# Performance work log

Measured on AMD Instinct MI355X. Metric: run time of the kernel, lower is better.

The kernel has to match this reference:

```python
import jax, jax.numpy as jnp
import numpy as np

N_NODES = 50000
N_EDGES = 800000
IN_DIM = 128
HEADS1, D1 = 4, 16   # hidden_dim // 4 = 16, concat -> 64
HID = HEADS1 * D1    # 64
OUT_DIM = 40
NEG_SLOPE = 0.2      # PyG GATConv default


def setup_inputs() -> dict:
    key = jax.random.key(0)
    ks = jax.random.split(key, 11)
    x = jax.random.normal(ks[0], (N_NODES, IN_DIM), dtype=jnp.float32)
    edge_index = jax.random.randint(ks[1], (2, N_EDGES), 0, N_NODES)
    s1 = 1.0 / np.sqrt(IN_DIM)
    s2 = 1.0 / np.sqrt(HID)
    return {
        "x": x,
        "edge_index": edge_index,
        "W1": jax.random.normal(ks[2], (IN_DIM, HEADS1 * D1), dtype=jnp.float32) * s1,
        "a_src1": jax.random.normal(ks[3], (HEADS1, D1), dtype=jnp.float32) * s2,
        "a_dst1": jax.random.normal(ks[4], (HEADS1, D1), dtype=jnp.float32) * s2,
        "b1": jnp.zeros((HID,), dtype=jnp.float32),
        "W2": jax.random.normal(ks[5], (HID, OUT_DIM), dtype=jnp.float32) * s2,
        "a_src2": jax.random.normal(ks[6], (1, OUT_DIM), dtype=jnp.float32) * s2,
        "a_dst2": jax.random.normal(ks[7], (1, OUT_DIM), dtype=jnp.float32) * s2,
        "b2": jnp.zeros((OUT_DIM,), dtype=jnp.float32),
    }


def gat_conv(x, src, dst, W, a_src, a_dst, b, heads, d, n_nodes):
    # linear projection, split into heads: [N, H, d]
    h = (x @ W).reshape(n_nodes, heads, d)
    # per-node attention logits: [N, H]
    alpha_src = jnp.einsum("nhd,hd->nh", h, a_src)
    alpha_dst = jnp.einsum("nhd,hd->nh", h, a_dst)
    # edge attention coefficients
    e = jax.nn.leaky_relu(alpha_src[src] + alpha_dst[dst], NEG_SLOPE)  # [E, H]
    # segment softmax over incoming edges of each destination node
    e_max = jax.ops.segment_max(e, dst, num_segments=n_nodes)
    e_max = jnp.where(jnp.isfinite(e_max), e_max, 0.0)
    e_exp = jnp.exp(e - e_max[dst])
    denom = jax.ops.segment_sum(e_exp, dst, num_segments=n_nodes)
    alpha = e_exp / (denom[dst] + 1e-16)  # [E, H]
    # weighted scatter-aggregate of source messages
    out = jax.ops.segment_sum(h[src] * alpha[..., None], dst, num_segments=n_nodes)
    return out.reshape(n_nodes, heads * d) + b


def reference(x, edge_index, W1, a_src1, a_dst1, b1, W2, a_src2, a_dst2, b2):
    n = x.shape[0]
    # PyG GATConv add_self_loops=True
    loop = jnp.arange(n, dtype=edge_index.dtype)
    src = jnp.concatenate([edge_index[0], loop])
    dst = jnp.concatenate([edge_index[1], loop])
    h = jax.nn.relu(gat_conv(x, src, dst, W1, a_src1, a_dst1, b1, HEADS1, D1, n))
    # dropout is identity in eval mode
    h = gat_conv(h, src, dst, W2, a_src2, a_dst2, b2, 1, OUT_DIM, n)
    return jax.nn.log_softmax(h, axis=1)
```

## Files before the change

kernel.cpp:

```cpp
#include <hip/hip_runtime.h>
#include <hip/hip_fp16.h>
#include <math.h>

#define NN    50000
#define NE0   800000
#define NE    850000
#define INDIM 128
#define HID   64
#define OUTD  40

#define NB    391
#define BSH   7
#define BCAP  3072

typedef unsigned short u16;
typedef unsigned char  u8;

__device__ inline u16 f2bf(float f) {
    unsigned u = __float_as_uint(f);
    return (u16)((u + 0x8000u) >> 16);
}
__device__ inline float bf2f(u16 h) {
    return __uint_as_float((unsigned)h << 16);
}

__global__ __launch_bounds__(512) void k_binit(int* __restrict__ bcur) {
    int i = threadIdx.x;
    if (i < NB) bcur[i] = i * BCAP;
}

__global__ __launch_bounds__(256) void k_bin(const int* __restrict__ ei,
                                             int* __restrict__ bcur,
                                             unsigned int* __restrict__ epack) {
    __shared__ int lh[NB];
    __shared__ int lbase[NB];
    const int tid = threadIdx.x;
    const int CH = (NE + 255) / 256;
    const int e_begin = blockIdx.x * CH;
    const int e_end = (e_begin + CH < NE) ? e_begin + CH : NE;

    for (int i = tid; i < NB; i += 256) lh[i] = 0;
    __syncthreads();
    for (int e = e_begin + tid; e < e_end; e += 256) {
        int dst = (e < NE0) ? ei[NE0 + e] : (e - NE0);
        atomicAdd(&lh[dst >> BSH], 1);
    }
    __syncthreads();
    for (int i = tid; i < NB; i += 256) {
        int c = lh[i];
        lbase[i] = c ? atomicAdd(&bcur[i], c) : 0;
        lh[i] = 0;
    }
    __syncthreads();
    for (int e = e_begin + tid; e < e_end; e += 256) {
        int src, dst;
        if (e < NE0) { src = ei[e]; dst = ei[NE0 + e]; }
        else         { src = e - NE0; dst = src; }
        int bkt = dst >> BSH;
        int lpos = atomicAdd(&lh[bkt], 1);
        epack[lbase[bkt] + lpos] = (unsigned int)src | ((unsigned int)(dst & 127) << 16);
    }
}

__global__ __launch_bounds__(256) void k_bucket_csr(
    const int* __restrict__ bcur, const unsigned int* __restrict__ epack,
    const float* __restrict__ asrc1, const float* __restrict__ adst1,
    int* __restrict__ off_s, int* __restrict__ off_e, int* __restrict__ esrc,
    u8* __restrict__ edst8, u16* __restrict__ w1u) {
    __shared__ int lh[128];
    __shared__ int lcur[128];
    __shared__ int sblk;
    __shared__ float sadst[512];
    const int tid = threadIdx.x, lane = tid & 63;
    const int b = blockIdx.x;
    const int e0 = b * BCAP;
    const int cnt = bcur[b] - e0;

    for (int i = tid; i < 512; i += 256) {
        int gi = b * 512 + i;
        sadst[i] = (gi < NN * 4) ? adst1[gi] : 0.f;
    }
    if (tid < 128) lh[tid] = 0;
    __syncthreads();
    for (int i = tid; i < cnt; i += 256)
        atomicAdd(&lh[epack[e0 + i] >> 16], 1);
    __syncthreads();

    int v = 0, incl = 0;
    if (tid < 128) {
        v = lh[tid];
        incl = v;
#pragma unroll
        for (int s = 1; s < 64; s <<= 1) {
            int t = __shfl_up(incl, s);
            if (lane >= s) incl += t;
        }
    }
    if (tid == 63) sblk = incl;
    __syncthreads();
    if (tid >= 64 && tid < 128) incl += sblk;
    if (tid < 128) {
        int ex = e0 + incl - v;
        lcur[tid] = ex;
        int gd = b * 128 + tid;
        if (gd < NN) { off_s[gd] = ex; off_e[gd] = ex + v; }
    }
    __syncthreads();

    for (int i = tid; i < cnt; i += 256) {
        unsigned int p = epack[e0 + i];
        int s  = (int)(p & 0xFFFFu);
        int dl = (int)(p >> 16);
        int pos = atomicAdd(&lcur[dl], 1);
        esrc[pos]  = s;
        edst8[pos] = (u8)dl;
        float4 av = *(const float4*)&asrc1[(size_t)s * 4];
        const float* ad = &sadst[dl * 4];
        float e0f = av.x + ad[0], e1f = av.y + ad[1];
        float e2f = av.z + ad[2], e3f = av.w + ad[3];
        e0f = (e0f > 0.f) ? e0f : 0.2f * e0f;
        e1f = (e1f > 0.f) ? e1f : 0.2f * e1f;
        e2f = (e2f > 0.f) ? e2f : 0.2f * e2f;
        e3f = (e3f > 0.f) ? e3f : 0.2f * e3f;
        unsigned lo = (unsigned)f2bf(__expf(e0f)) | ((unsigned)f2bf(__expf(e1f)) << 16);
        unsigned hi = (unsigned)f2bf(__expf(e2f)) | ((unsigned)f2bf(__expf(e3f)) << 16);
        *(uint2*)&w1u[(size_t)pos * 4] = make_uint2(lo, hi);
    }
}

__global__ __launch_bounds__(256) void k_w2(
    const int* __restrict__ bcur, const int* __restrict__ esrc,
    const u8* __restrict__ edst8, const float* __restrict__ asrc2,
    const float* __restrict__ adst2, u16* __restrict__ w2u) {
    __shared__ float sadst[128];
    const int tid = threadIdx.x;
    const int b = blockIdx.x;
    const int e0 = b * BCAP, e1 = bcur[b];
    if (tid < 128) {
        int gd = b * 128 + tid;
        sadst[tid] = (gd < NN) ? adst2[gd] : 0.f;
    }
    __syncthreads();
    for (int i = e0 + tid; i < e1; i += 256) {
        int s = esrc[i];
        float e = asrc2[s] + sadst[edst8[i]];
        e = (e > 0.f) ? e : 0.2f * e;
        w2u[i] = f2bf(__expf(e));
    }
}

__global__ __launch_bounds__(256, 2) void k_gemm1(
    const float* __restrict__ x, const float* __restrict__ W1,
    const float* __restrict__ a_s, const float* __restrict__ a_d,
    __half* __restrict__ h1h, float* __restrict__ asrc1, float* __restrict__ adst1)
{
    __shared__ float Wl[INDIM * HID];
    __shared__ float xs[64 * 132];
    const int tid = threadIdx.x;
    const int r0 = blockIdx.x * 64;

    const float4* W4 = (const float4*)W1;
    float4* Wl4 = (float4*)Wl;
#pragma unroll
    for (int i = 0; i < 8; ++i) Wl4[tid + i * 256] = W4[tid + i * 256];

    const float4* x4 = (const float4*)x;
#pragma unroll
    for (int i = 0; i < 8; ++i) {
        int idx = tid + i * 256;
        int row = idx >> 5;
        int k4  = idx & 31;
        int nr = r0 + row;
        float4 v = make_float4(0.f, 0.f, 0.f, 0.f);
        if (nr < NN) v = x4[(size_t)nr * 32 + k4];
        *(float4*)&xs[row * 132 + k4 * 4] = v;
    }
    __syncthreads();

    const int rg = tid >> 4;
    const int cg = tid & 15;
    const int c4 = cg * 4;
    const float as0 = a_s[c4], as1v = a_s[c4+1], as2v = a_s[c4+2], as3v = a_s[c4+3];
    const float ad0 = a_d[c4], ad1v = a_d[c4+1], ad2v = a_d[c4+2], ad3v = a_d[c4+3];

    float acc[4][4];
#pragma unroll
    for (int i = 0; i < 4; ++i)
#pragma unroll
        for (int j = 0; j < 4; ++j) acc[i][j] = 0.f;

#pragma unroll 4
    for (int k4 = 0; k4 < 32; ++k4) {
        float4 xv[4];
#pragma unroll
        for (int i = 0; i < 4; ++i)
            xv[i] = *(const float4*)&xs[(rg * 4 + i) * 132 + k4 * 4];
        const float* wp = &Wl[(k4 * 4) * HID + c4];
        float4 w0 = *(const float4*)(wp);
        float4 w1 = *(const float4*)(wp + HID);
        float4 w2 = *(const float4*)(wp + 2 * HID);
        float4 w3 = *(const float4*)(wp + 3 * HID);
#pragma unroll
        for (int i = 0; i < 4; ++i) {
            acc[i][0] += xv[i].x * w0.x + xv[i].y * w1.x + xv[i].z * w2.x + xv[i].w * w3.x;
            acc[i][1] += xv[i].x * w0.y + xv[i].y * w1.y + xv[i].z * w2.y + xv[i].w * w3.y;
            acc[i][2] += xv[i].x * w0.z + xv[i].y * w1.z + xv[i].z * w2.z + xv[i].w * w3.z;
            acc[i][3] += xv[i].x * w0.w + xv[i].y * w1.w + xv[i].z * w2.w + xv[i].w * w3.w;
        }
    }

#pragma unroll
    for (int i = 0; i < 4; ++i) {
        const int n = r0 + rg * 4 + i;
        if (n < NN) {
            __half2 ha = __floats2half2_rn(acc[i][0], acc[i][1]);
            __half2 hb = __floats2half2_rn(acc[i][2], acc[i][3]);
            *(__half2*)&h1h[(size_t)n * HID + c4]     = ha;
            *(__half2*)&h1h[(size_t)n * HID + c4 + 2] = hb;
        }
        float ps = acc[i][0] * as0 + acc[i][1] * as1v + acc[i][2] * as2v + acc[i][3] * as3v;
        float pd = acc[i][0] * ad0 + acc[i][1] * ad1v + acc[i][2] * ad2v + acc[i][3] * ad3v;
        ps += __shfl_xor(ps, 1); ps += __shfl_xor(ps, 2);
        pd += __shfl_xor(pd, 1); pd += __shfl_xor(pd, 2);
        if ((cg & 3) == 0 && n < NN) {
            int head = cg >> 2;
            asrc1[n * 4 + head] = ps;
            adst1[n * 4 + head] = pd;
        }
    }
}

__global__ __launch_bounds__(256) void k_fagg1(
    const int* __restrict__ off_s, const int* __restrict__ off_e,
    const int* __restrict__ esrc, const u16* __restrict__ w1u,
    const __half* __restrict__ h1h, const float* __restrict__ b1,
    float* __restrict__ hmid)
{
    const int wv = threadIdx.x >> 6, lane = threadIdx.x & 63;
    const int g = lane >> 5, li = lane & 31;
    const int n = blockIdx.x * 8 + wv * 2 + g;
    const int s0 = off_s[n], s1 = off_e[n];
    const int hp = li >> 3;
    const int last = s1 - 1;

    int maxc = s1 - s0;
    maxc = max(maxc, __shfl_xor(maxc, 32));

    float l = 0.f, a0 = 0.f, a1 = 0.f;
    const char* h1b = (const char*)h1h;
    for (int t = 0; t < maxc; t += 8) {
        int   sx[8];
        float wx[8];
#pragma unroll
        for (int j = 0; j < 8; ++j) {
            int ix  = s0 + t + j;
            int ixc = (ix < s1) ? ix : last;
            sx[j] = esrc[ixc];
            float w = bf2f(w1u[(size_t)ixc * 4 + hp]);
            wx[j] = (ix < s1) ? w : 0.f;
        }
        float2 hx[8];
#pragma unroll
        for (int j = 0; j < 8; ++j) {
            __half2 hv = *(const __half2*)(h1b + ((size_t)sx[j] * 128 + li * 4));
            hx[j] = __half22float2(hv);
        }
#pragma unroll
        for (int j = 0; j < 8; ++j) {
            l  += wx[j];
            a0 += wx[j] * hx[j].x;
            a1 += wx[j] * hx[j].y;
        }
    }
    float2 bv = *(const float2*)&b1[li * 2];
    float rcp = 1.f / l;
    float2 o;
    o.x = fmaxf(a0 * rcp + bv.x, 0.f);
    o.y = fmaxf(a1 * rcp + bv.y, 0.f);
    *(float2*)&hmid[(size_t)n * HID + li * 2] = o;
}

__global__ __launch_bounds__(320) void k_gemm2(
    const float* __restrict__ hin, const float* __restrict__ W2,
    const float* __restrict__ a_s, const float* __restrict__ a_d,
    __half* __restrict__ h2h, float* __restrict__ asrc2, float* __restrict__ adst2)
{
    __shared__ float Wl[HID * OUTD];
    __shared__ float xs[32 * 68];
    __shared__ float s_as[32], s_ad[32];
    const int tid = threadIdx.x;
    const int r0 = blockIdx.x * 32;

    const float4* W4 = (const float4*)W2;
    float4* Wl4 = (float4*)Wl;
    for (int i = tid; i < 640; i += 320) Wl4[i] = W4[i];
    const float4* x4 = (const float4*)hin;
    for (int i = tid; i < 512; i += 320) {
        int row = i >> 4;
        int k4  = i & 15;
        int nr = r0 + row;
        float4 v = make_float4(0.f, 0.f, 0.f, 0.f);
        if (nr < NN) v = x4[(size_t)nr * 16 + k4];
        *(float4*)&xs[row * 68 + k4 * 4] = v;
    }
    if (tid < 32) { s_as[tid] = 0.f; s_ad[tid] = 0.f; }
    __syncthreads();

    const int r  = tid / 10;
    const int cg = tid % 10;
    const int c4 = cg * 4;
    float a0 = 0.f, a1 = 0.f, a2 = 0.f, a3 = 0.f;
#pragma unroll 4
    for (int k4 = 0; k4 < 16; ++k4) {
        float4 xv = *(const float4*)&xs[r * 68 + k4 * 4];
        const float* wp = &Wl[(k4 * 4) * OUTD + c4];
        float4 w0 = *(const float4*)(wp);
        float4 w1 = *(const float4*)(wp + OUTD);
        float4 w2 = *(const float4*)(wp + 2 * OUTD);
        float4 w3 = *(const float4*)(wp + 3 * OUTD);
        a0 += xv.x * w0.x + xv.y * w1.x + xv.z * w2.x + xv.w * w3.x;
        a1 += xv.x * w0.y + xv.y * w1.y + xv.z * w2.y + xv.w * w3.y;
        a2 += xv.x * w0.z + xv.y * w1.z + xv.z * w2.z + xv.w * w3.z;
        a3 += xv.x * w0.w + xv.y * w1.w + xv.z * w2.w + xv.w * w3.w;
    }
    const int n = r0 + r;
    float ps = a0 * a_s[c4] + a1 * a_s[c4 + 1] + a2 * a_s[c4 + 2] + a3 * a_s[c4 + 3];
    float pd = a0 * a_d[c4] + a1 * a_d[c4 + 1] + a2 * a_d[c4 + 2] + a3 * a_d[c4 + 3];
    atomicAdd(&s_as[r], ps);
    atomicAdd(&s_ad[r], pd);
    if (n < NN) {
        __half2 ha = __floats2half2_rn(a0, a1);
        __half2 hb = __floats2half2_rn(a2, a3);
        *(__half2*)&h2h[(size_t)n * OUTD + c4]     = ha;
        *(__half2*)&h2h[(size_t)n * OUTD + c4 + 2] = hb;
    }
    __syncthreads();
    if (tid < 32) {
        int n2 = r0 + tid;
        if (n2 < NN) { asrc2[n2] = s_as[tid]; adst2[n2] = s_ad[tid]; }
    }
}

__global__ __launch_bounds__(256) void k_fagg2(
    const int* __restrict__ off_s, const int* __restrict__ off_e,
    const int* __restrict__ esrc, const u16* __restrict__ w2u,
    const __half* __restrict__ h2h, const float* __restrict__ b2,
    float* __restrict__ out)
{
    __shared__ float svals[12][OUTD];
    const int wv = threadIdx.x >> 6, lane = threadIdx.x & 63;
    const int g = lane / 20;
    const int li = lane - g * 20;
    const bool ga = (g < 3);
    const int n = blockIdx.x * 12 + wv * 3 + (ga ? g : 0);
    const bool valid = ga && (n < NN);
    const int nc = valid ? n : 0;
    const int s0 = off_s[nc], s1 = off_e[nc];
    const int last = s1 - 1;

    int maxc = valid ? (s1 - s0) : 0;
#pragma unroll
    for (int o = 1; o < 64; o <<= 1) maxc = max(maxc, __shfl_xor(maxc, o));

    float l = 0.f, a0 = 0.f, a1 = 0.f;
    const char* h2b = (const char*)h2h;
    for (int t = 0; t < maxc; t += 8) {
        int   sx[8];
        float wx[8];
#pragma unroll
        for (int j = 0; j < 8; ++j) {
            int ix  = s0 + t + j;
            int ixc = (ix < s1) ? ix : last;
            sx[j] = esrc[ixc];
            float w = bf2f(w2u[ixc]);
            wx[j] = (ix < s1) ? w : 0.f;
        }
        float2 hx[8];
#pragma unroll
        for (int j = 0; j < 8; ++j) {
            __half2 hv = *(const __half2*)(h2b + ((size_t)sx[j] * 80 + li * 4));
            hx[j] = __half22float2(hv);
        }
#pragma unroll
        for (int j = 0; j < 8; ++j) {
            l  += wx[j];
            a0 += wx[j] * hx[j].x;
            a1 += wx[j] * hx[j].y;
        }
    }
    if (valid) {
        float rcp = 1.f / l;
        float2 bv = *(const float2*)&b2[li * 2];
        svals[wv * 3 + g][li * 2]     = a0 * rcp + bv.x;
        svals[wv * 3 + g][li * 2 + 1] = a1 * rcp + bv.y;
    }
    __syncthreads();

    for (int r = wv; r < 12; r += 4) {
        int n2 = blockIdx.x * 12 + r;
        if (n2 >= NN) continue;
        float v = (lane < OUTD) ? svals[r][lane] : -1e30f;
        float mx = v;
#pragma unroll
        for (int o = 32; o; o >>= 1) mx = fmaxf(mx, __shfl_xor(mx, o));
        float ex = (lane < OUTD) ? __expf(v - mx) : 0.f;
        float sm = ex;
#pragma unroll
        for (int o = 32; o; o >>= 1) sm += __shfl_xor(sm, o);
        if (lane < OUTD) out[(size_t)n2 * OUTD + lane] = v - mx - __logf(sm);
    }
}

extern "C" void kernel_launch(void* const* d_in, const int* in_sizes, int n_in,
                              void* d_out, int out_size, void* d_ws, size_t ws_size,
                              hipStream_t stream)
{
    const float* x   = (const float*)d_in[0];
    const int*   ei  = (const int*)  d_in[1];
    const float* W1  = (const float*)d_in[2];
    const float* as1 = (const float*)d_in[3];
    const float* ad1 = (const float*)d_in[4];
    const float* b1  = (const float*)d_in[5];
    const float* W2  = (const float*)d_in[6];
    const float* as2 = (const float*)d_in[7];
    const float* ad2 = (const float*)d_in[8];
    const float* b2  = (const float*)d_in[9];
    float* out = (float*)d_out;

    char* ws = (char*)d_ws;
    __half* h1h   = (__half*)(ws);
    float*  hmid  = (float*) (ws + 6400000);
    unsigned int* epack = (unsigned int*)(ws + 6400000);
    u16*    w1u   = (u16*)   (ws + 19200000);
    __half* h2h   = (__half*)(ws + 19200000);
    float*  asrc2 = (float*) (ws + 23200000);
    float*  adst2 = (float*) (ws + 23400000);
    u16*    w2u   = (u16*)   (ws + 23600000);
    float*  asrc1 = (float*) (ws + 28809216);
    float*  adst1 = (float*) (ws + 29609216);
    int*    off_s = (int*)   (ws + 30409216);
    int*    off_e = (int*)   (ws + 30609216);
    int*    esrc  = (int*)   (ws + 30809216);
    u8*     edst8 = (u8*)    (ws + 35613824);
    int*    bcur  = (int*)   (ws + 36814976);

    hipLaunchKernelGGL(k_binit,      dim3(1),    dim3(512), 0, stream, bcur);
    hipLaunchKernelGGL(k_bin,        dim3(256),  dim3(256), 0, stream, ei, bcur, epack);
    hipLaunchKernelGGL(k_gemm1,      dim3(782),  dim3(256), 0, stream, x, W1, as1, ad1, h1h, asrc1, adst1);
    hipLaunchKernelGGL(k_bucket_csr, dim3(NB),   dim3(256), 0, stream, bcur, epack, asrc1, adst1, off_s, off_e, esrc, edst8, w1u);
    hipLaunchKernelGGL(k_fagg1,      dim3(6250), dim3(256), 0, stream, off_s, off_e, esrc, w1u, h1h, b1, hmid);
    hipLaunchKernelGGL(k_gemm2,      dim3(1563), dim3(320), 0, stream, hmid, W2, as2, ad2, h2h, asrc2, adst2);
    hipLaunchKernelGGL(k_w2,         dim3(NB),   dim3(256), 0, stream, bcur, esrc, edst8, asrc2, adst2, w2u);
    hipLaunchKernelGGL(k_fagg2,      dim3(4167), dim3(256), 0, stream, off_s, off_e, esrc, w2u, h2h, b2, out);
}
```

Baseline: 208.4 us.

## Fuse layer-2 edge weights into aggregation and pack edge records

Removes the separate k_w2 kernel: layer-2 attention weights are now computed on the fly inside k_fagg2 from asrc2/adst2, which adds a gather per edge but drops one kernel launch and a pass over the edges. Layer-1 edge data (src plus four bf16 weights) is packed into one 16-byte record, so k_fagg1 issues a single vector load per edge instead of two loads. The record is padded with an unused dst field, which raises the bytes read per edge. k_bin also uses half as many blocks, each handling a larger chunk.

Measured after the change: 212.6 us. 1.02x slower.

```diff
diff --git a/kernel.cpp b/kernel.cpp
--- a/kernel.cpp
+++ b/kernel.cpp
@@ -35,7 +35,7 @@
     __shared__ int lh[NB];
     __shared__ int lbase[NB];
     const int tid = threadIdx.x;
-    const int CH = (NE + 255) / 256;
+    const int CH = (NE + 127) / 128;
     const int e_begin = blockIdx.x * CH;
     const int e_end = (e_begin + CH < NE) ? e_begin + CH : NE;
 
@@ -65,8 +65,8 @@
 __global__ __launch_bounds__(256) void k_bucket_csr(
     const int* __restrict__ bcur, const unsigned int* __restrict__ epack,
     const float* __restrict__ asrc1, const float* __restrict__ adst1,
-    int* __restrict__ off_s, int* __restrict__ off_e, int* __restrict__ esrc,
-    u8* __restrict__ edst8, u16* __restrict__ w1u) {
+    int* __restrict__ off_s, int* __restrict__ off_e,
+    uint4* __restrict__ erec, int* __restrict__ esrc) {
     __shared__ int lh[128];
     __shared__ int lcur[128];
     __shared__ int sblk;
@@ -112,8 +112,6 @@
         int s  = (int)(p & 0xFFFFu);
         int dl = (int)(p >> 16);
         int pos = atomicAdd(&lcur[dl], 1);
-        esrc[pos]  = s;
-        edst8[pos] = (u8)dl;
         float4 av = *(const float4*)&asrc1[(size_t)s * 4];
         const float* ad = &sadst[dl * 4];
         float e0f = av.x + ad[0], e1f = av.y + ad[1];
@@ -124,28 +122,8 @@
         e3f = (e3f > 0.f) ? e3f : 0.2f * e3f;
         unsigned lo = (unsigned)f2bf(__expf(e0f)) | ((unsigned)f2bf(__expf(e1f)) << 16);
         unsigned hi = (unsigned)f2bf(__expf(e2f)) | ((unsigned)f2bf(__expf(e3f)) << 16);
-        *(uint2*)&w1u[(size_t)pos * 4] = make_uint2(lo, hi);
-    }
-}
-
-__global__ __launch_bounds__(256) void k_w2(
-    const int* __restrict__ bcur, const int* __restrict__ esrc,
-    const u8* __restrict__ edst8, const float* __restrict__ asrc2,
-    const float* __restrict__ adst2, u16* __restrict__ w2u) {
-    __shared__ float sadst[128];
-    const int tid = threadIdx.x;
-    const int b = blockIdx.x;
-    const int e0 = b * BCAP, e1 = bcur[b];
-    if (tid < 128) {
-        int gd = b * 128 + tid;
-        sadst[tid] = (gd < NN) ? adst2[gd] : 0.f;
-    }
-    __syncthreads();
-    for (int i = e0 + tid; i < e1; i += 256) {
-        int s = esrc[i];
-        float e = asrc2[s] + sadst[edst8[i]];
-        e = (e > 0.f) ? e : 0.2f * e;
-        w2u[i] = f2bf(__expf(e));
+        erec[pos] = make_uint4((unsigned)s, lo, hi, (unsigned)dl);
+        esrc[pos] = s;
     }
 }
 
@@ -232,7 +210,7 @@
 
 __global__ __launch_bounds__(256) void k_fagg1(
     const int* __restrict__ off_s, const int* __restrict__ off_e,
-    const int* __restrict__ esrc, const u16* __restrict__ w1u,
+    const uint4* __restrict__ erec,
     const __half* __restrict__ h1h, const float* __restrict__ b1,
     float* __restrict__ hmid)
 {
@@ -249,20 +227,22 @@
     float l = 0.f, a0 = 0.f, a1 = 0.f;
     const char* h1b = (const char*)h1h;
     for (int t = 0; t < maxc; t += 8) {
-        int   sx[8];
+        uint4 er[8];
         float wx[8];
 #pragma unroll
         for (int j = 0; j < 8; ++j) {
             int ix  = s0 + t + j;
             int ixc = (ix < s1) ? ix : last;
-            sx[j] = esrc[ixc];
-            float w = bf2f(w1u[(size_t)ixc * 4 + hp]);
+            er[j] = erec[ixc];
+            unsigned pair = (hp & 2) ? er[j].z : er[j].y;
+            unsigned wb = (hp & 1) ? (pair >> 16) : (pair & 0xFFFFu);
+            float w = bf2f((u16)wb);
             wx[j] = (ix < s1) ? w : 0.f;
         }
         float2 hx[8];
 #pragma unroll
         for (int j = 0; j < 8; ++j) {
-            __half2 hv = *(const __half2*)(h1b + ((size_t)sx[j] * 128 + li * 4));
+            __half2 hv = *(const __half2*)(h1b + ((size_t)er[j].x * 128 + li * 4));
             hx[j] = __half22float2(hv);
         }
 #pragma unroll
@@ -343,7 +323,8 @@
 
 __global__ __launch_bounds__(256) void k_fagg2(
     const int* __restrict__ off_s, const int* __restrict__ off_e,
-    const int* __restrict__ esrc, const u16* __restrict__ w2u,
+    const int* __restrict__ esrc, const float* __restrict__ asrc2,
+    const float* __restrict__ adst2,
     const __half* __restrict__ h2h, const float* __restrict__ b2,
     float* __restrict__ out)
 {
@@ -357,6 +338,7 @@
     const int nc = valid ? n : 0;
     const int s0 = off_s[nc], s1 = off_e[nc];
     const int last = s1 - 1;
+    const float adst = adst2[nc];
 
     int maxc = valid ? (s1 - s0) : 0;
 #pragma unroll
@@ -365,16 +347,18 @@
     float l = 0.f, a0 = 0.f, a1 = 0.f;
     const char* h2b = (const char*)h2h;
     for (int t = 0; t < maxc; t += 8) {
-        int   sx[8];
-        float wx[8];
+        int sx[8];
+        int ok[8];
 #pragma unroll
         for (int j = 0; j < 8; ++j) {
             int ix  = s0 + t + j;
-            int ixc = (ix < s1) ? ix : last;
+            ok[j] = (ix < s1);
+            int ixc = ok[j] ? ix : last;
             sx[j] = esrc[ixc];
-            float w = bf2f(w2u[ixc]);
-            wx[j] = (ix < s1) ? w : 0.f;
-        }
+        }
+        float ax[8];
+#pragma unroll
+        for (int j = 0; j < 8; ++j) ax[j] = asrc2[sx[j]];
         float2 hx[8];
 #pragma unroll
         for (int j = 0; j < 8; ++j) {
@@ -383,9 +367,13 @@
         }
 #pragma unroll
         for (int j = 0; j < 8; ++j) {
-            l  += wx[j];
-            a0 += wx[j] * hx[j].x;
-            a1 += wx[j] * hx[j].y;
+            float e = ax[j] + adst;
+            e = (e > 0.f) ? e : 0.2f * e;
+            float w = __expf(e);
+            w = ok[j] ? w : 0.f;
+            l  += w;
+            a0 += w * hx[j].x;
+            a1 += w * hx[j].y;
         }
     }
     if (valid) {
@@ -429,27 +417,24 @@
 
     char* ws = (char*)d_ws;
     __half* h1h   = (__half*)(ws);
-    float*  hmid  = (float*) (ws + 6400000);
-    unsigned int* epack = (unsigned int*)(ws + 6400000);
-    u16*    w1u   = (u16*)   (ws + 19200000);
+    float*  hmid  = (float*) (ws +  6400000);
     __half* h2h   = (__half*)(ws + 19200000);
-    float*  asrc2 = (float*) (ws + 23200000);
-    float*  adst2 = (float*) (ws + 23400000);
-    u16*    w2u   = (u16*)   (ws + 23600000);
-    float*  asrc1 = (float*) (ws + 28809216);
-    float*  adst1 = (float*) (ws + 29609216);
-    int*    off_s = (int*)   (ws + 30409216);
-    int*    off_e = (int*)   (ws + 30609216);
-    int*    esrc  = (int*)   (ws + 30809216);
-    u8*     edst8 = (u8*)    (ws + 35613824);
-    int*    bcur  = (int*)   (ws + 36814976);
+    float*  asrc1 = (float*) (ws + 23200000);
+    float*  adst1 = (float*) (ws + 24000000);
+    float*  asrc2 = (float*) (ws + 24800000);
+    float*  adst2 = (float*) (ws + 25000000);
+    int*    off_s = (int*)   (ws + 25200000);
+    int*    off_e = (int*)   (ws + 25400000);
+    unsigned int* epack = (unsigned int*)(ws + 25600000);
+    uint4*  erec  = (uint4*) (ws + 30404608);
+    int*    esrc  = (int*)   (ws + 49623040);
+    int*    bcur  = (int*)   (ws + 54427648);
 
     hipLaunchKernelGGL(k_binit,      dim3(1),    dim3(512), 0, stream, bcur);
-    hipLaunchKernelGGL(k_bin,        dim3(256),  dim3(256), 0, stream, ei, bcur, epack);
+    hipLaunchKernelGGL(k_bin,        dim3(128),  dim3(256), 0, stream, ei, bcur, epack);
     hipLaunchKernelGGL(k_gemm1,      dim3(782),  dim3(256), 0, stream, x, W1, as1, ad1, h1h, asrc1, adst1);
-    hipLaunchKernelGGL(k_bucket_csr, dim3(NB),   dim3(256), 0, stream, bcur, epack, asrc1, adst1, off_s, off_e, esrc, edst8, w1u);
-    hipLaunchKernelGGL(k_fagg1,      dim3(6250), dim3(256), 0, stream, off_s, off_e, esrc, w1u, h1h, b1, hmid);
+    hipLaunchKernelGGL(k_bucket_csr, dim3(NB),   dim3(256), 0, stream, bcur, epack, asrc1, adst1, off_s, off_e, erec, esrc);
+    hipLaunchKernelGGL(k_fagg1,      dim3(6250), dim3(256), 0, stream, off_s, off_e, erec, h1h, b1, hmid);
     hipLaunchKernelGGL(k_gemm2,      dim3(1563), dim3(320), 0, stream, hmid, W2, as2, ad2, h2h, asrc2, adst2);
-    hipLaunchKernelGGL(k_w2,         dim3(NB),   dim3(256), 0, stream, bcur, esrc, edst8, asrc2, adst2, w2u);
-    hipLaunchKernelGGL(k_fagg2,      dim3(4167), dim3(256), 0, stream, off_s, off_e, esrc, w2u, h2h, b2, out);
-}
+    hipLaunchKernelGGL(k_fagg2,      dim3(4167), dim3(256), 0, stream, off_s, off_e, esrc, asrc2, adst2, h2h, b2, out);
+}
```

## Cache edges in LDS during binning, widen aggregation lanes, store hidden in fp16

Applied to the files above, without the earlier changes.

The binning kernel now keeps each block's edge records in shared memory during the histogram pass, so edge_index is read from global memory once instead of twice. Both aggregation kernels move from 2 to 4 features per lane, so each node uses half as many lanes and each block covers twice as many nodes. The per-wavefront max-degree loop bound becomes a per-group loop bound. The intermediate hidden layer is stored as fp16 instead of fp32, halving that write and the read in the second GEMM, and the workspace is re-laid out to match. The cost is more lane divergence within a wavefront on the variable-length edge loops, fewer lanes per gather, and some rounding from the fp16 hidden layer.

Measured after the change: 208.0 us. Within noise of the previous version (-0.2%).

```diff
diff --git a/kernel.cpp b/kernel.cpp
--- a/kernel.cpp
+++ b/kernel.cpp
@@ -34,16 +34,23 @@
                                              unsigned int* __restrict__ epack) {
     __shared__ int lh[NB];
     __shared__ int lbase[NB];
+    __shared__ unsigned ebuf[3328];
     const int tid = threadIdx.x;
     const int CH = (NE + 255) / 256;
-    const int e_begin = blockIdx.x * CH;
-    const int e_end = (e_begin + CH < NE) ? e_begin + CH : NE;
+    const int e0 = blockIdx.x * CH;
+    const int e1 = (e0 + CH < NE) ? e0 + CH : NE;
+    const int cnt = e1 - e0;
 
     for (int i = tid; i < NB; i += 256) lh[i] = 0;
     __syncthreads();
-    for (int e = e_begin + tid; e < e_end; e += 256) {
-        int dst = (e < NE0) ? ei[NE0 + e] : (e - NE0);
-        atomicAdd(&lh[dst >> BSH], 1);
+    for (int i = tid; i < cnt; i += 256) {
+        int e = e0 + i;
+        int src, dst;
+        if (e < NE0) { src = ei[e]; dst = ei[NE0 + e]; }
+        else         { src = e - NE0; dst = src; }
+        int bkt = dst >> BSH;
+        ebuf[i] = (unsigned)src | ((unsigned)(dst & 127) << 16) | ((unsigned)bkt << 23);
+        atomicAdd(&lh[bkt], 1);
     }
     __syncthreads();
     for (int i = tid; i < NB; i += 256) {
@@ -52,13 +59,11 @@
         lh[i] = 0;
     }
     __syncthreads();
-    for (int e = e_begin + tid; e < e_end; e += 256) {
-        int src, dst;
-        if (e < NE0) { src = ei[e]; dst = ei[NE0 + e]; }
-        else         { src = e - NE0; dst = src; }
-        int bkt = dst >> BSH;
+    for (int i = tid; i < cnt; i += 256) {
+        unsigned rec = ebuf[i];
+        int bkt = rec >> 23;
         int lpos = atomicAdd(&lh[bkt], 1);
-        epack[lbase[bkt] + lpos] = (unsigned int)src | ((unsigned int)(dst & 127) << 16);
+        epack[lbase[bkt] + lpos] = rec & 0x7FFFFFu;
     }
 }
 
@@ -234,54 +239,60 @@
     const int* __restrict__ off_s, const int* __restrict__ off_e,
     const int* __restrict__ esrc, const u16* __restrict__ w1u,
     const __half* __restrict__ h1h, const float* __restrict__ b1,
-    float* __restrict__ hmid)
+    __half* __restrict__ hmid)
 {
     const int wv = threadIdx.x >> 6, lane = threadIdx.x & 63;
-    const int g = lane >> 5, li = lane & 31;
-    const int n = blockIdx.x * 8 + wv * 2 + g;
+    const int g = lane >> 4, li = lane & 15;
+    const int n = blockIdx.x * 16 + wv * 4 + g;
     const int s0 = off_s[n], s1 = off_e[n];
-    const int hp = li >> 3;
+    const int hp = li >> 2;
     const int last = s1 - 1;
 
-    int maxc = s1 - s0;
-    maxc = max(maxc, __shfl_xor(maxc, 32));
-
-    float l = 0.f, a0 = 0.f, a1 = 0.f;
-    const char* h1b = (const char*)h1h;
-    for (int t = 0; t < maxc; t += 8) {
+    float l = 0.f, a0 = 0.f, a1 = 0.f, a2 = 0.f, a3 = 0.f;
+    const char* hb = (const char*)h1h;
+    for (int t = s0; t < s1; t += 8) {
         int   sx[8];
         float wx[8];
 #pragma unroll
         for (int j = 0; j < 8; ++j) {
-            int ix  = s0 + t + j;
+            int ix  = t + j;
             int ixc = (ix < s1) ? ix : last;
             sx[j] = esrc[ixc];
             float w = bf2f(w1u[(size_t)ixc * 4 + hp]);
             wx[j] = (ix < s1) ? w : 0.f;
         }
-        float2 hx[8];
-#pragma unroll
-        for (int j = 0; j < 8; ++j) {
-            __half2 hv = *(const __half2*)(h1b + ((size_t)sx[j] * 128 + li * 4));
-            hx[j] = __half22float2(hv);
+        float2 f0[8], f1[8];
+#pragma unroll
+        for (int j = 0; j < 8; ++j) {
+            uint2 raw = *(const uint2*)(hb + ((size_t)sx[j] * 128 + li * 8));
+            f0[j] = __half22float2(*(__half2*)&raw.x);
+            f1[j] = __half22float2(*(__half2*)&raw.y);
         }
 #pragma unroll
         for (int j = 0; j < 8; ++j) {
             l  += wx[j];
-            a0 += wx[j] * hx[j].x;
-            a1 += wx[j] * hx[j].y;
-        }
-    }
-    float2 bv = *(const float2*)&b1[li * 2];
+            a0 += wx[j] * f0[j].x;
+            a1 += wx[j] * f0[j].y;
+            a2 += wx[j] * f1[j].x;
+            a3 += wx[j] * f1[j].y;
+        }
+    }
     float rcp = 1.f / l;
-    float2 o;
-    o.x = fmaxf(a0 * rcp + bv.x, 0.f);
-    o.y = fmaxf(a1 * rcp + bv.y, 0.f);
-    *(float2*)&hmid[(size_t)n * HID + li * 2] = o;
+    float4 bv = *(const float4*)&b1[li * 4];
+    float o0 = fmaxf(a0 * rcp + bv.x, 0.f);
+    float o1 = fmaxf(a1 * rcp + bv.y, 0.f);
+    float o2 = fmaxf(a2 * rcp + bv.z, 0.f);
+    float o3 = fmaxf(a3 * rcp + bv.w, 0.f);
+    __half2 ha = __floats2half2_rn(o0, o1);
+    __half2 hc = __floats2half2_rn(o2, o3);
+    uint2 st;
+    st.x = *(unsigned*)&ha;
+    st.y = *(unsigned*)&hc;
+    *(uint2*)((char*)hmid + ((size_t)n * 128 + li * 8)) = st;
 }
 
 __global__ __launch_bounds__(320) void k_gemm2(
-    const float* __restrict__ hin, const float* __restrict__ W2,
+    const __half* __restrict__ hin, const float* __restrict__ W2,
     const float* __restrict__ a_s, const float* __restrict__ a_d,
     __half* __restrict__ h2h, float* __restrict__ asrc2, float* __restrict__ adst2)
 {
@@ -294,14 +305,19 @@
     const float4* W4 = (const float4*)W2;
     float4* Wl4 = (float4*)Wl;
     for (int i = tid; i < 640; i += 320) Wl4[i] = W4[i];
-    const float4* x4 = (const float4*)hin;
+    const uint2* x4 = (const uint2*)hin;
     for (int i = tid; i < 512; i += 320) {
         int row = i >> 4;
-        int k4  = i & 15;
+        int c   = i & 15;
         int nr = r0 + row;
         float4 v = make_float4(0.f, 0.f, 0.f, 0.f);
-        if (nr < NN) v = x4[(size_t)nr * 16 + k4];
-        *(float4*)&xs[row * 68 + k4 * 4] = v;
+        if (nr < NN) {
+            uint2 raw = x4[(size_t)nr * 16 + c];
+            float2 p0 = __half22float2(*(__half2*)&raw.x);
+            float2 p1 = __half22float2(*(__half2*)&raw.y);
+            v = make_float4(p0.x, p0.y, p1.x, p1.y);
+        }
+        *(float4*)&xs[row * 68 + c * 4] = v;
     }
     if (tid < 32) { s_as[tid] = 0.f; s_ad[tid] = 0.f; }
     __syncthreads();
@@ -347,57 +363,59 @@
     const __half* __restrict__ h2h, const float* __restrict__ b2,
     float* __restrict__ out)
 {
-    __shared__ float svals[12][OUTD];
+    __shared__ float svals[24][OUTD];
     const int wv = threadIdx.x >> 6, lane = threadIdx.x & 63;
-    const int g = lane / 20;
-    const int li = lane - g * 20;
-    const bool ga = (g < 3);
-    const int n = blockIdx.x * 12 + wv * 3 + (ga ? g : 0);
+    const int g = lane / 10;
+    const int li = lane - g * 10;
+    const bool ga = (g < 6);
+    const int n = blockIdx.x * 24 + wv * 6 + (ga ? g : 0);
     const bool valid = ga && (n < NN);
-    const int nc = valid ? n : 0;
-    const int s0 = off_s[nc], s1 = off_e[nc];
+    const int s0 = valid ? off_s[n] : 0;
+    const int s1 = valid ? off_e[n] : 0;
     const int last = s1 - 1;
 
-    int maxc = valid ? (s1 - s0) : 0;
-#pragma unroll
-    for (int o = 1; o < 64; o <<= 1) maxc = max(maxc, __shfl_xor(maxc, o));
-
-    float l = 0.f, a0 = 0.f, a1 = 0.f;
-    const char* h2b = (const char*)h2h;
-    for (int t = 0; t < maxc; t += 8) {
+    float l = 0.f, a0 = 0.f, a1 = 0.f, a2 = 0.f, a3 = 0.f;
+    const char* hb = (const char*)h2h;
+    for (int t = s0; t < s1; t += 8) {
         int   sx[8];
         float wx[8];
 #pragma unroll
         for (int j = 0; j < 8; ++j) {
-            int ix  = s0 + t + j;
+            int ix  = t + j;
             int ixc = (ix < s1) ? ix : last;
             sx[j] = esrc[ixc];
             float w = bf2f(w2u[ixc]);
             wx[j] = (ix < s1) ? w : 0.f;
         }
-        float2 hx[8];
-#pragma unroll
-        for (int j = 0; j < 8; ++j) {
-            __half2 hv = *(const __half2*)(h2b + ((size_t)sx[j] * 80 + li * 4));
-            hx[j] = __half22float2(hv);
+        float2 f0[8], f1[8];
+#pragma unroll
+        for (int j = 0; j < 8; ++j) {
+            uint2 raw = *(const uint2*)(hb + ((size_t)sx[j] * 80 + li * 8));
+            f0[j] = __half22float2(*(__half2*)&raw.x);
+            f1[j] = __half22float2(*(__half2*)&raw.y);
         }
 #pragma unroll
         for (int j = 0; j < 8; ++j) {
             l  += wx[j];
-            a0 += wx[j] * hx[j].x;
-            a1 += wx[j] * hx[j].y;
+            a0 += wx[j] * f0[j].x;
+            a1 += wx[j] * f0[j].y;
+            a2 += wx[j] * f1[j].x;
+            a3 += wx[j] * f1[j].y;
         }
     }
     if (valid) {
         float rcp = 1.f / l;
-        float2 bv = *(const float2*)&b2[li * 2];
-        svals[wv * 3 + g][li * 2]     = a0 * rcp + bv.x;
-        svals[wv * 3 + g][li * 2 + 1] = a1 * rcp + bv.y;
-    }
-    __syncthreads();
-
-    for (int r = wv; r < 12; r += 4) {
-        int n2 = blockIdx.x * 12 + r;
+        float4 bv = *(const float4*)&b2[li * 4];
+        int r = wv * 6 + g;
+        svals[r][li * 4]     = a0 * rcp + bv.x;
+        svals[r][li * 4 + 1] = a1 * rcp + bv.y;
+        svals[r][li * 4 + 2] = a2 * rcp + bv.z;
+        svals[r][li * 4 + 3] = a3 * rcp + bv.w;
+    }
+    __syncthreads();
+
+    for (int r = wv; r < 24; r += 4) {
+        int n2 = blockIdx.x * 24 + r;
         if (n2 >= NN) continue;
         float v = (lane < OUTD) ? svals[r][lane] : -1e30f;
         float mx = v;
@@ -429,27 +447,27 @@
 
     char* ws = (char*)d_ws;
     __half* h1h   = (__half*)(ws);
-    float*  hmid  = (float*) (ws + 6400000);
-    unsigned int* epack = (unsigned int*)(ws + 6400000);
-    u16*    w1u   = (u16*)   (ws + 19200000);
-    __half* h2h   = (__half*)(ws + 19200000);
-    float*  asrc2 = (float*) (ws + 23200000);
-    float*  adst2 = (float*) (ws + 23400000);
-    u16*    w2u   = (u16*)   (ws + 23600000);
-    float*  asrc1 = (float*) (ws + 28809216);
-    float*  adst1 = (float*) (ws + 29609216);
-    int*    off_s = (int*)   (ws + 30409216);
-    int*    off_e = (int*)   (ws + 30609216);
-    int*    esrc  = (int*)   (ws + 30809216);
-    u8*     edst8 = (u8*)    (ws + 35613824);
-    int*    bcur  = (int*)   (ws + 36814976);
+    __half* hmidh = (__half*)(ws +  6400000);
+    __half* h2h   = (__half*)(ws + 12800000);
+    float*  asrc1 = (float*) (ws + 16800000);
+    float*  adst1 = (float*) (ws + 17600000);
+    float*  asrc2 = (float*) (ws + 18400000);
+    float*  adst2 = (float*) (ws + 18600000);
+    int*    off_s = (int*)   (ws + 18800000);
+    int*    off_e = (int*)   (ws + 19000000);
+    unsigned int* epack = (unsigned int*)(ws + 19200000);
+    int*    esrc  = (int*)   (ws + 24004608);
+    u8*     edst8 = (u8*)    (ws + 28809216);
+    u16*    w1u   = (u16*)   (ws + 30010368);
+    u16*    w2u   = (u16*)   (ws + 39619584);
+    int*    bcur  = (int*)   (ws + 42021888);
 
     hipLaunchKernelGGL(k_binit,      dim3(1),    dim3(512), 0, stream, bcur);
     hipLaunchKernelGGL(k_bin,        dim3(256),  dim3(256), 0, stream, ei, bcur, epack);
     hipLaunchKernelGGL(k_gemm1,      dim3(782),  dim3(256), 0, stream, x, W1, as1, ad1, h1h, asrc1, adst1);
     hipLaunchKernelGGL(k_bucket_csr, dim3(NB),   dim3(256), 0, stream, bcur, epack, asrc1, adst1, off_s, off_e, esrc, edst8, w1u);
-    hipLaunchKernelGGL(k_fagg1,      dim3(6250), dim3(256), 0, stream, off_s, off_e, esrc, w1u, h1h, b1, hmid);
-    hipLaunchKernelGGL(k_gemm2,      dim3(1563), dim3(320), 0, stream, hmid, W2, as2, ad2, h2h, asrc2, adst2);
+    hipLaunchKernelGGL(k_fagg1,      dim3(3125), dim3(256), 0, stream, off_s, off_e, esrc, w1u, h1h, b1, hmidh);
+    hipLaunchKernelGGL(k_gemm2,      dim3(1563), dim3(320), 0, stream, hmidh, W2, as2, ad2, h2h, asrc2, adst2);
     hipLaunchKernelGGL(k_w2,         dim3(NB),   dim3(256), 0, stream, bcur, esrc, edst8, asrc2, adst2, w2u);
-    hipLaunchKernelGGL(k_fagg2,      dim3(4167), dim3(256), 0, stream, off_s, off_e, esrc, w2u, h2h, b2, out);
-}
+    hipLaunchKernelGGL(k_fagg2,      dim3(2084), dim3(256), 0, stream, off_s, off_e, esrc, w2u, h2h, b2, out);
+}
```
